# Optimization experiments

Hardware: AMD Instinct MI355X
Metric: run time of the kernel (lower is better)

The kernel has to match this reference:

```python
import jax, jax.numpy as jnp
import numpy as np

N = 50000      # nodes
E = 800000     # edges (avg degree 16)
DIN = 512      # input_dim
DH = 256       # hidden_dim
KMAX = 50      # max_clusters; K = max(5, min(50, ceil(N/50))) = 50 for N=50000


def _gcn_propagate(h, src, dst, n):
    """Symmetric-normalized GCN aggregation with self-loops (PyG GCNConv).
    h: already linearly transformed node features (n, d)."""
    loop = jnp.arange(n)
    s = jnp.concatenate([src, loop])
    d = jnp.concatenate([dst, loop])
    deg = jax.ops.segment_sum(jnp.ones_like(d, dtype=h.dtype), d, num_segments=n)
    dinv = jnp.where(deg > 0, deg ** -0.5, 0.0)
    norm = dinv[s] * dinv[d]                      # (E+N,)
    return jax.ops.segment_sum(norm[:, None] * h[s], d, num_segments=n)


def setup_inputs() -> dict:
    key = jax.random.key(0)
    ks = jax.random.split(key, 6)
    x = jax.random.normal(ks[0], (N, DIN), dtype=jnp.float32)
    edge_index = jax.random.randint(ks[1], (2, E), 0, N, dtype=jnp.int64)
    positions = jax.random.uniform(ks[2], (N, 2), dtype=jnp.float32)
    # GCNConv params (glorot-ish weights, zero bias as in PyG init)
    W1 = jax.random.normal(ks[3], (DIN, DH), dtype=jnp.float32) * np.float32(1.0 / np.sqrt(DIN))
    b1 = jnp.zeros((DH,), dtype=jnp.float32)
    W2 = jax.random.normal(ks[4], (DH, KMAX), dtype=jnp.float32) * np.float32(1.0 / np.sqrt(DH))
    b2 = jnp.zeros((KMAX,), dtype=jnp.float32)
    spatial_weight = jnp.asarray(1.0, dtype=jnp.float32)
    return {"x": x, "positions": positions, "W1": W1, "b1": b1,
            "W2": W2, "b2": b2, "spatial_weight": spatial_weight,
            "edge_index": edge_index}


def reference(x, positions, W1, b1, W2, b2, spatial_weight, edge_index):
    src, dst = edge_index[0], edge_index[1]
    n = x.shape[0]
    # layer 1: GCNConv(input_dim -> hidden_dim) + ReLU
    h = jax.nn.relu(_gcn_propagate(x @ W1, src, dst, n) + b1)
    # layer 2: GCNConv(hidden_dim -> max_clusters)
    s = _gcn_propagate(h @ W2, src, dst, n) + b2
    # K = max(5, min(50, ceil(N/50))) = 50 here -> s[:, :K] is identity slice
    S = jax.nn.softmax(s[:, :KMAX], axis=1)       # (N, K), Eq. 7
    # spatial loss (Eq. 9): softmax > 0 always, so the >0 guards are no-ops
    d2 = jnp.sum((positions[src] - positions[dst]) ** 2, axis=1)   # (E,) squared dist
    dot = jnp.sum(S[src] * S[dst], axis=1)                          # (E,) sum_k S_ik S_jk
    L_spatial = spatial_weight * jnp.sum(d2 * dot) / src.shape[0]
    return S, L_spatial
```

## Files before the change

kernel.cpp:

```cpp
#include <hip/hip_runtime.h>
#include <math.h>


typedef __attribute__((ext_vector_type(8))) short bf16x8;
typedef __attribute__((ext_vector_type(4))) float f32x4;
typedef __attribute__((ext_vector_type(4))) unsigned int u32x4;
typedef _Float16 f16;
typedef __attribute__((ext_vector_type(2))) _Float16 f16x2;
typedef __attribute__((ext_vector_type(4))) _Float16 f16x4;
typedef __attribute__((ext_vector_type(8))) _Float16 f16x8;

__device__ inline unsigned short f32_to_bf16(float f) {
    unsigned u = __float_as_uint(f);
    unsigned r = u + 0x7FFFu + ((u >> 16) & 1u);
    return (unsigned short)(r >> 16);
}
__device__ inline float bf16_to_f32(unsigned short h) {
    return __uint_as_float((unsigned)h << 16);
}

__device__ inline void glds16(const void* g, void* l) {
    __builtin_amdgcn_global_load_lds(
        (const __attribute__((address_space(1))) unsigned int*)g,
        (__attribute__((address_space(3))) unsigned int*)l, 16, 0, 0);
}

__global__ void detect_i64_kernel(const unsigned* __restrict__ w, int* __restrict__ flag) {
    __shared__ int red[256];
    int cnt = 0;
    for (int i = threadIdx.x; i < 4096; i += 256)
        cnt += (w[2 * i + 1] == 0u) ? 1 : 0;
    red[threadIdx.x] = cnt;
    __syncthreads();
    for (int s = 128; s > 0; s >>= 1) {
        if ((int)threadIdx.x < s) red[threadIdx.x] += red[threadIdx.x + s];
        __syncthreads();
    }
    if (threadIdx.x == 0) *flag = (red[0] > 2048) ? 1 : 0;
}

__global__ void convert_edges_kernel(const void* __restrict__ ei, int* __restrict__ es,
                                     int* __restrict__ ed, int* __restrict__ cnt,
                                     int E, const int* __restrict__ flag) {
    int idx = blockIdx.x * blockDim.x + threadIdx.x;
    if (idx >= 2 * E) return;
    int v;
    if (*flag) v = (int)((const long long*)ei)[idx];
    else       v = ((const int*)ei)[idx];
    if (idx < E) es[idx] = v;
    else { ed[idx - E] = v; atomicAdd(&cnt[v], 1); }
}

__global__ __launch_bounds__(1024) void scan_block_kernel(const int* __restrict__ cnt,
        int* __restrict__ row_ptr, int* __restrict__ btot, int n) {
    __shared__ int buf[1024];
    int i = blockIdx.x * 1024 + threadIdx.x;
    buf[threadIdx.x] = (i < n) ? cnt[i] : 0;
    __syncthreads();
    for (int off = 1; off < 1024; off <<= 1) {
        int t = ((int)threadIdx.x >= off) ? buf[threadIdx.x - off] : 0;
        __syncthreads();
        buf[threadIdx.x] += t;
        __syncthreads();
    }
    if (i < n) row_ptr[i + 1] = buf[threadIdx.x];
    if (threadIdx.x == 1023) btot[blockIdx.x] = buf[1023];
}

__global__ __launch_bounds__(1024) void scan_tops_kernel(int* __restrict__ btot, int nb) {
    __shared__ int buf[1024];
    buf[threadIdx.x] = ((int)threadIdx.x < nb) ? btot[threadIdx.x] : 0;
    __syncthreads();
    for (int off = 1; off < 1024; off <<= 1) {
        int t = ((int)threadIdx.x >= off) ? buf[threadIdx.x - off] : 0;
        __syncthreads();
        buf[threadIdx.x] += t;
        __syncthreads();
    }
    if ((int)threadIdx.x < nb) btot[threadIdx.x] = buf[threadIdx.x];
}

__global__ void scan_finalize_kernel(int* __restrict__ row_ptr, const int* __restrict__ btot,
        const int* __restrict__ cnt, int* __restrict__ cursor, float* __restrict__ dinv, int n) {
    int i = blockIdx.x * blockDim.x + threadIdx.x;
    if (i >= n) return;
    int blk = i >> 10;
    int off = blk ? btot[blk - 1] : 0;
    int incl = row_ptr[i + 1] + off;
    row_ptr[i + 1] = incl;
    cursor[i] = incl - cnt[i];
    dinv[i] = rsqrtf((float)(cnt[i] + 1));
    if (i == 0) row_ptr[0] = 0;
}

__global__ void scatter_kernel(const int* __restrict__ es, const int* __restrict__ ed,
                               const float* __restrict__ dinv, int* __restrict__ cursor,
                               int* __restrict__ csr_src, float* __restrict__ csr_nrm, int E) {
    int e = blockIdx.x * blockDim.x + threadIdx.x;
    if (e < E) {
        int s = es[e];
        int d = ed[e];
        int p = atomicAdd(&cursor[d], 1);
        csr_src[p] = s;
        csr_nrm[p] = dinv[s];
    }
}

__global__ void wsplit_kernel(const float* __restrict__ W,
                              unsigned short* __restrict__ Th,
                              unsigned short* __restrict__ Tl, int K, int N, int nk) {
    int idx = blockIdx.x * 256 + threadIdx.x;
    if (idx >= K * N) return;
    int k = idx / N, n = idx % N;
    float f = W[idx];
    unsigned short h = f32_to_bf16(f);
    unsigned short l = f32_to_bf16(f - bf16_to_f32(h));
    int p = n >> 7, np = n & 127, t = k >> 5, kg = (k & 31) >> 3, ke = k & 7;
    size_t o = ((size_t)((p * nk + t) * 4 + kg) << 10) + np * 8 + ke;
    Th[o] = h;
    Tl[o] = l;
}

__global__ void wsplit2_kernel(const float* __restrict__ W2,
                               f16* __restrict__ W2t_hi, f16* __restrict__ W2t_lo,
                               int K, int NC) {
    int idx = blockIdx.x * 256 + threadIdx.x;
    if (idx >= 64 * K) return;
    int n = idx / K, k = idx % K;
    float v = (n < NC) ? W2[(size_t)k * NC + n] : 0.f;
    f16 h = (f16)v;
    W2t_hi[idx] = h;
    W2t_lo[idx] = (f16)(v - (float)h);
}

#define G1_BM 128
#define G1_BN 128
#define G1_BK 32

__global__ __launch_bounds__(256) void gemm1_mfma(
        const float* __restrict__ X, const unsigned short* __restrict__ WtH,
        const unsigned short* __restrict__ WtL, f16* __restrict__ C,
        int M, int K, int N) {
    __shared__ __align__(16) unsigned char lds[32768];

    const int tid  = threadIdx.x;
    const int lane = tid & 63;
    const int wave = tid >> 6;
    const int wm   = wave & 1;
    const int wn   = wave >> 1;
    const int m0   = blockIdx.x * G1_BM;
    const int pn   = blockIdx.y;
    const int nk   = K / G1_BK;

    const float* Xbase[4];
    #pragma unroll
    for (int i = 0; i < 4; ++i) {
        int c   = i * 256 + tid;
        int row = c >> 3;
        int sl  = (c & 7) ^ (row & 7);
        int gr  = m0 + row;
        if (gr > M - 1) gr = M - 1;
        Xbase[i] = X + (size_t)gr * K + sl * 4;
    }
    const unsigned short* BhBase = WtH + ((size_t)pn * nk << 12) + (size_t)tid * 8;
    const unsigned short* BlBase = WtL + ((size_t)pn * nk << 12) + (size_t)tid * 8;

    f32x4 acc[4][4] = {};
    const int kq   = lane >> 4;
    const int frow = lane & 15;
    const int bOff = 16384 + (kq << 11) + ((wn * 64 + frow) << 4);

    for (int t = 0; t < nk; ++t) {
        const int k0 = t * G1_BK;
        #pragma unroll
        for (int i = 0; i < 4; ++i)
            glds16(Xbase[i] + k0, lds + i * 4096 + wave * 1024);
        const unsigned short* bh = BhBase + (size_t)t * 4096;
        const unsigned short* bl = BlBase + (size_t)t * 4096;
        glds16(bh,        lds + 16384 + wave * 1024);
        glds16(bh + 2048, lds + 20480 + wave * 1024);
        glds16(bl,        lds + 24576 + wave * 1024);
        glds16(bl + 2048, lds + 28672 + wave * 1024);
        __syncthreads();

        bf16x8 bhf[4], blf[4];
        #pragma unroll
        for (int nn = 0; nn < 4; ++nn) {
            bhf[nn] = *(const bf16x8*)(lds + bOff + nn * 256);
            blf[nn] = *(const bf16x8*)(lds + bOff + 8192 + nn * 256);
        }
        #pragma unroll
        for (int mm = 0; mm < 4; ++mm) {
            int ra = wm * 64 + mm * 16 + frow;
            int rb = ra << 7;
            int sw = (ra & 7) << 4;
            int s0 = kq << 1;
            f32x4 p0 = *(const f32x4*)(lds + rb + ((s0 << 4) ^ sw));
            f32x4 p1 = *(const f32x4*)(lds + rb + (((s0 + 1) << 4) ^ sw));
            float f[8] = {p0[0], p0[1], p0[2], p0[3], p1[0], p1[1], p1[2], p1[3]};
            u32x4 hv, lv;
            #pragma unroll
            for (int p = 0; p < 4; ++p) {
                unsigned b0 = __float_as_uint(f[2 * p]);
                unsigned b1 = __float_as_uint(f[2 * p + 1]);
                hv[p] = __builtin_amdgcn_perm(b1, b0, 0x07060302u);
                float l0 = f[2 * p]     - __uint_as_float(b0 & 0xFFFF0000u);
                float l1 = f[2 * p + 1] - __uint_as_float(b1 & 0xFFFF0000u);
                lv[p] = __builtin_amdgcn_perm(__float_as_uint(l1),
                                              __float_as_uint(l0), 0x07060302u);
            }
            union { u32x4 u; bf16x8 b; } ah, al;
            ah.u = hv; al.u = lv;
            #pragma unroll
            for (int nn = 0; nn < 4; ++nn)
                acc[mm][nn] = __builtin_amdgcn_mfma_f32_16x16x32_bf16(ah.b, bhf[nn], acc[mm][nn], 0, 0, 0);
            #pragma unroll
            for (int nn = 0; nn < 4; ++nn)
                acc[mm][nn] = __builtin_amdgcn_mfma_f32_16x16x32_bf16(ah.b, blf[nn], acc[mm][nn], 0, 0, 0);
            #pragma unroll
            for (int nn = 0; nn < 4; ++nn)
                acc[mm][nn] = __builtin_amdgcn_mfma_f32_16x16x32_bf16(al.b, bhf[nn], acc[mm][nn], 0, 0, 0);
        }
        __syncthreads();
    }

    const int n0 = pn * G1_BN;
    #pragma unroll
    for (int mm = 0; mm < 4; ++mm) {
        #pragma unroll
        for (int i = 0; i < 4; ++i) {
            int gr = m0 + wm * 64 + mm * 16 + kq * 4 + i;
            if (gr >= M) continue;
            #pragma unroll
            for (int nn = 0; nn < 4; ++nn) {
                int gc = n0 + wn * 64 + nn * 16 + frow;
                C[(size_t)gr * N + gc] = (f16)acc[mm][nn][i];
            }
        }
    }
}

__global__ __launch_bounds__(256) void agg1_gemm2_kernel(
        const f16* __restrict__ h0, const float* __restrict__ dinv,
        const int* __restrict__ row_ptr, const int* __restrict__ csr_src,
        const float* __restrict__ csr_nrm, const float* __restrict__ b1,
        const f16* __restrict__ W2t_hi, const f16* __restrict__ W2t_lo,
        f16* __restrict__ g, int n, int K, int KC) {
    __shared__ __align__(16) f16 hs[32][264];

    const int tid  = threadIdx.x;
    const int lane = tid & 63;
    const int wave = tid >> 6;
    const int base = blockIdx.x * 32;
    const int c    = lane & 31;
    const int hf   = lane >> 5;

    const f16x8* h0v8 = (const f16x8*)h0;

    float4 bA = ((const float4*)b1)[c * 2];
    float4 bB = ((const float4*)b1)[c * 2 + 1];
    float bb[8] = {bA.x, bA.y, bA.z, bA.w, bB.x, bB.y, bB.z, bB.w};

    for (int i = 0; i < 8; ++i) {
        int wid = base + wave * 8 + i;
        float acc[8] = {};
        if (wid < n) {
            float di = dinv[wid];
            f16x8 vs = h0v8[(size_t)wid * 32 + c];
            float selfm = (hf == 0) ? di * di : 0.f;
            #pragma unroll
            for (int q = 0; q < 8; ++q) acc[q] = selfm * (float)vs[q];
            int beg = row_ptr[wid], end = row_ptr[wid + 1];
            int j = beg;
            for (; j + 4 <= end; j += 4) {
                int   sA = csr_src[j + hf];
                int   sB = csr_src[j + 2 + hf];
                float nA = csr_nrm[j + hf] * di;
                float nB = csr_nrm[j + 2 + hf] * di;
                f16x8 uA = h0v8[(size_t)sA * 32 + c];
                f16x8 uB = h0v8[(size_t)sB * 32 + c];
                #pragma unroll
                for (int q = 0; q < 8; ++q) acc[q] = fmaf(nA, (float)uA[q], acc[q]);
                #pragma unroll
                for (int q = 0; q < 8; ++q) acc[q] = fmaf(nB, (float)uB[q], acc[q]);
            }
            for (; j < end; j += 2) {
                int  jj = j + hf;
                bool vld = jj < end;
                int   sA = csr_src[vld ? jj : j];
                float nA = vld ? csr_nrm[jj] * di : 0.f;
                f16x8 uA = h0v8[(size_t)sA * 32 + c];
                #pragma unroll
                for (int q = 0; q < 8; ++q) acc[q] = fmaf(nA, (float)uA[q], acc[q]);
            }
        }
        #pragma unroll
        for (int q = 0; q < 8; ++q) acc[q] += __shfl_xor(acc[q], 32);
        if (hf == 0) {
            f16x8 o;
            #pragma unroll
            for (int q = 0; q < 8; ++q)
                o[q] = (wid < n) ? (f16)fmaxf(acc[q] + bb[q], 0.f) : (f16)0.f;
            *(f16x8*)&hs[wave * 8 + i][c * 8] = o;
        }
    }
    __syncthreads();

    const int wm   = wave & 1;
    const int wn   = wave >> 1;
    const int kq   = lane >> 4;
    const int frow = lane & 15;
    const int koff = kq * 8;

    f32x4 acc2[2] = {};
    const f16* bh_base[2];
    const f16* bl_base[2];
    #pragma unroll
    for (int nn = 0; nn < 2; ++nn) {
        int r = wn * 32 + nn * 16 + frow;
        bh_base[nn] = W2t_hi + (size_t)r * K + koff;
        bl_base[nn] = W2t_lo + (size_t)r * K + koff;
    }

    for (int t = 0; t < K / 32; ++t) {
        const int kk = t * 32;
        f16x8 a = *(const f16x8*)&hs[wm * 16 + frow][kk + koff];
        #pragma unroll
        for (int nn = 0; nn < 2; ++nn) {
            f16x8 bh = *(const f16x8*)(bh_base[nn] + kk);
            f16x8 bl = *(const f16x8*)(bl_base[nn] + kk);
            acc2[nn] = __builtin_amdgcn_mfma_f32_16x16x32_f16(a, bh, acc2[nn], 0, 0, 0);
            acc2[nn] = __builtin_amdgcn_mfma_f32_16x16x32_f16(a, bl, acc2[nn], 0, 0, 0);
        }
    }

    #pragma unroll
    for (int i = 0; i < 4; ++i) {
        int gr = base + wm * 16 + kq * 4 + i;
        if (gr >= n) continue;
        #pragma unroll
        for (int nn = 0; nn < 2; ++nn) {
            int gc = wn * 32 + nn * 16 + frow;
            if (gc < KC) g[(size_t)gr * KC + gc] = (f16)acc2[nn][i];
        }
    }
}

__global__ __launch_bounds__(256) void agg2_softmax_kernel(const f16* __restrict__ g,
        const float* __restrict__ dinv, const int* __restrict__ row_ptr,
        const int* __restrict__ csr_src, const float* __restrict__ csr_nrm,
        const float* __restrict__ b2, float* __restrict__ S, f16* __restrict__ Sh,
        int n, int KC) {
    int wid = (int)((blockIdx.x * (size_t)blockDim.x + threadIdx.x) >> 6);
    int lane = threadIdx.x & 63;
    if (wid >= n) return;
    bool act = lane < KC;
    size_t gidx = act ? (size_t)lane : 0;
    float di = dinv[wid];
    float a0 = 0.f, a1 = 0.f, a2 = 0.f, a3 = 0.f;
    if (act) a0 = di * di * (float)g[(size_t)wid * KC + lane];
    int beg = row_ptr[wid], end = row_ptr[wid + 1];
    int j = beg;
    for (; j + 4 <= end; j += 4) {
        int s0 = csr_src[j], s1 = csr_src[j + 1], s2 = csr_src[j + 2], s3 = csr_src[j + 3];
        float n0 = csr_nrm[j]     * di;
        float n1 = csr_nrm[j + 1] * di;
        float n2 = csr_nrm[j + 2] * di;
        float n3 = csr_nrm[j + 3] * di;
        float g0 = (float)g[(size_t)s0 * KC + gidx];
        float g1 = (float)g[(size_t)s1 * KC + gidx];
        float g2 = (float)g[(size_t)s2 * KC + gidx];
        float g3 = (float)g[(size_t)s3 * KC + gidx];
        a0 = fmaf(n0, g0, a0);
        a1 = fmaf(n1, g1, a1);
        a2 = fmaf(n2, g2, a2);
        a3 = fmaf(n3, g3, a3);
    }
    for (; j < end; ++j) {
        int s0 = csr_src[j];
        float n0 = csr_nrm[j] * di;
        a0 = fmaf(n0, (float)g[(size_t)s0 * KC + gidx], a0);
    }
    float acc = (a0 + a1) + (a2 + a3);
    float val = act ? (acc + b2[lane]) : -INFINITY;
    float m = val;
    #pragma unroll
    for (int o = 32; o > 0; o >>= 1) m = fmaxf(m, __shfl_xor(m, o));
    float e = act ? expf(val - m) : 0.f;
    float ssum = e;
    #pragma unroll
    for (int o = 32; o > 0; o >>= 1) ssum += __shfl_xor(ssum, o);
    {
        float sv = act ? (e / ssum) : 0.f;
        if (act) S[(size_t)wid * KC + lane] = sv;
        Sh[(size_t)wid * 64 + lane] = (f16)sv;
    }
}

__global__ __launch_bounds__(256) void loss_partial_kernel(const int* __restrict__ es,
        const int* __restrict__ ed, const float* __restrict__ pos,
        const f16* __restrict__ Sh, float* __restrict__ parts, int E) {
    float local = 0.f;
    int stride = gridDim.x * blockDim.x;
    for (int e = blockIdx.x * blockDim.x + threadIdx.x; e < E; e += stride) {
        int s = es[e], d = ed[e];
        float2 ps = ((const float2*)pos)[s];
        float2 pd = ((const float2*)pos)[d];
        float dx = ps.x - pd.x, dy = ps.y - pd.y;
        float d2 = dx * dx + dy * dy;
        const f16x8* Sa = (const f16x8*)(Sh + (size_t)s * 64);
        const f16x8* Sb = (const f16x8*)(Sh + (size_t)d * 64);
        float dot = 0.f;
        #pragma unroll
        for (int q = 0; q < 7; ++q) {
            f16x8 a = Sa[q], b = Sb[q];
            #pragma unroll
            for (int k = 0; k < 8; ++k)
                dot = fmaf((float)a[k], (float)b[k], dot);
        }
        local = fmaf(d2, dot, local);
    }
    __shared__ float red[256];
    red[threadIdx.x] = local;
    __syncthreads();
    for (int s = 128; s > 0; s >>= 1) {
        if ((int)threadIdx.x < s) red[threadIdx.x] += red[threadIdx.x + s];
        __syncthreads();
    }
    if (threadIdx.x == 0) parts[blockIdx.x] = red[0];
}

__global__ __launch_bounds__(1024) void loss_final_kernel(const float* __restrict__ parts,
        const float* __restrict__ sw, float* __restrict__ out, float invE) {
    __shared__ float red[1024];
    red[threadIdx.x] = parts[threadIdx.x];
    __syncthreads();
    for (int s = 512; s > 0; s >>= 1) {
        if ((int)threadIdx.x < s) red[threadIdx.x] += red[threadIdx.x + s];
        __syncthreads();
    }
    if (threadIdx.x == 0) out[0] = sw[0] * red[0] * invE;
}

extern "C" void kernel_launch(void* const* d_in, const int* in_sizes, int n_in,
                              void* d_out, int out_size, void* d_ws, size_t ws_size,
                              hipStream_t stream) {
    const float* x   = (const float*)d_in[0];
    const float* pos = (const float*)d_in[1];
    const float* W1  = (const float*)d_in[2];
    const float* b1  = (const float*)d_in[3];
    const float* W2  = (const float*)d_in[4];
    const float* b2  = (const float*)d_in[5];
    const float* sw  = (const float*)d_in[6];
    const void*  ei  = d_in[7];

    const int DH  = in_sizes[3];
    const int KC  = in_sizes[5];
    const int DIN = in_sizes[2] / DH;
    const int n   = in_sizes[0] / DIN;
    const int E   = in_sizes[7] / 2;

    char* p = (char*)d_ws;
    auto alloc = [&](size_t bytes) {
        char* r = p;
        p += (bytes + 255) & ~(size_t)255;
        return r;
    };
    int*   flag    = (int*)alloc(256);
    int*   es      = (int*)alloc((size_t)E * 4);
    int*   ed      = (int*)alloc((size_t)E * 4);
    int*   cnt     = (int*)alloc((size_t)n * 4);
    int*   cursor  = (int*)alloc((size_t)n * 4);
    int*   row_ptr = (int*)alloc(((size_t)n + 1) * 4);
    int*   btot    = (int*)alloc(1024 * 4);
    int*   csr     = (int*)alloc((size_t)E * 4);
    float* csr_nrm = (float*)alloc((size_t)E * 4);
    float* dinv    = (float*)alloc((size_t)n * 4);
    float* parts   = (float*)alloc(1024 * 4);
    unsigned short* Wt_hi = (unsigned short*)alloc((size_t)DIN * DH * 2);
    unsigned short* Wt_lo = (unsigned short*)alloc((size_t)DIN * DH * 2);
    f16*   W2t_hi  = (f16*)alloc((size_t)64 * DH * 2);
    f16*   W2t_lo  = (f16*)alloc((size_t)64 * DH * 2);
    f16*   h0      = (f16*)alloc((size_t)n * DH * 2);
    f16*   g       = (f16*)alloc((size_t)n * KC * 2);
    f16*   Sh      = (f16*)alloc((size_t)n * 64 * 2);

    float* S    = (float*)d_out;
    float* Lout = S + (size_t)n * KC;

    const int nb = (n + 1023) / 1024;
    const int nk = DIN / G1_BK;

    hipMemsetAsync(cnt, 0, (size_t)n * 4, stream);
    detect_i64_kernel<<<1, 256, 0, stream>>>((const unsigned*)ei, flag);
    convert_edges_kernel<<<(2 * E + 255) / 256, 256, 0, stream>>>(ei, es, ed, cnt, E, flag);
    scan_block_kernel<<<nb, 1024, 0, stream>>>(cnt, row_ptr, btot, n);
    scan_tops_kernel<<<1, 1024, 0, stream>>>(btot, nb);
    scan_finalize_kernel<<<(n + 255) / 256, 256, 0, stream>>>(row_ptr, btot, cnt, cursor, dinv, n);
    scatter_kernel<<<(E + 255) / 256, 256, 0, stream>>>(es, ed, dinv, cursor, csr, csr_nrm, E);

    wsplit_kernel<<<(DIN * DH + 255) / 256, 256, 0, stream>>>(W1, Wt_hi, Wt_lo, DIN, DH, nk);
    wsplit2_kernel<<<(64 * DH + 255) / 256, 256, 0, stream>>>(W2, W2t_hi, W2t_lo, DH, KC);

    dim3 g1((n + G1_BM - 1) / G1_BM, DH / G1_BN);
    gemm1_mfma<<<g1, 256, 0, stream>>>(x, Wt_hi, Wt_lo, h0, n, DIN, DH);

    agg1_gemm2_kernel<<<(n + 31) / 32, 256, 0, stream>>>(
        h0, dinv, row_ptr, csr, csr_nrm, b1, W2t_hi, W2t_lo, g, n, DH, KC);

    agg2_softmax_kernel<<<(int)(((size_t)n * 64 + 255) / 256), 256, 0, stream>>>(
        g, dinv, row_ptr, csr, csr_nrm, b2, S, Sh, n, KC);

    loss_partial_kernel<<<1024, 256, 0, stream>>>(es, ed, pos, Sh, parts, E);
    loss_final_kernel<<<1, 1024, 0, stream>>>(parts, sw, Lout, 1.0f / (float)E);
}
```

Before: 326.8 us.

## Interleave CSR src/norm, pad layer-2 features to 64, vectorize loss

Packs each CSR entry's source index and normalization weight into one int2 so a single load fetches both in the aggregation kernels. Pads the layer-2 intermediate to a 64-column stride, which removes per-lane bounds masking, and unrolls the layer-2 gather by eight for more memory-level parallelism. The loss kernel processes two edges per iteration with vector index loads and computes the softmax dot product with packed half-precision multiplies. The half-precision accumulation in the loss dot product lowers accuracy compared with the previous fp32 FMA chain.

New measurement: 334.8 us. 2.5% more time.

```diff
diff --git a/kernel.cpp b/kernel.cpp
--- a/kernel.cpp
+++ b/kernel.cpp
@@ -95,14 +95,13 @@
 
 __global__ void scatter_kernel(const int* __restrict__ es, const int* __restrict__ ed,
                                const float* __restrict__ dinv, int* __restrict__ cursor,
-                               int* __restrict__ csr_src, float* __restrict__ csr_nrm, int E) {
+                               int2* __restrict__ csr_sn, int E) {
     int e = blockIdx.x * blockDim.x + threadIdx.x;
     if (e < E) {
         int s = es[e];
         int d = ed[e];
         int p = atomicAdd(&cursor[d], 1);
-        csr_src[p] = s;
-        csr_nrm[p] = dinv[s];
+        csr_sn[p] = make_int2(s, __float_as_int(dinv[s]));
     }
 }
 
@@ -242,8 +241,8 @@
 
 __global__ __launch_bounds__(256) void agg1_gemm2_kernel(
         const f16* __restrict__ h0, const float* __restrict__ dinv,
-        const int* __restrict__ row_ptr, const int* __restrict__ csr_src,
-        const float* __restrict__ csr_nrm, const float* __restrict__ b1,
+        const int* __restrict__ row_ptr, const int2* __restrict__ csr_sn,
+        const float* __restrict__ b1,
         const f16* __restrict__ W2t_hi, const f16* __restrict__ W2t_lo,
         f16* __restrict__ g, int n, int K, int KC) {
     __shared__ __align__(16) f16 hs[32][264];
@@ -273,12 +272,12 @@
             int beg = row_ptr[wid], end = row_ptr[wid + 1];
             int j = beg;
             for (; j + 4 <= end; j += 4) {
-                int   sA = csr_src[j + hf];
-                int   sB = csr_src[j + 2 + hf];
-                float nA = csr_nrm[j + hf] * di;
-                float nB = csr_nrm[j + 2 + hf] * di;
-                f16x8 uA = h0v8[(size_t)sA * 32 + c];
-                f16x8 uB = h0v8[(size_t)sB * 32 + c];
+                int2 eA = csr_sn[j + hf];
+                int2 eB = csr_sn[j + 2 + hf];
+                float nA = __int_as_float(eA.y) * di;
+                float nB = __int_as_float(eB.y) * di;
+                f16x8 uA = h0v8[(size_t)eA.x * 32 + c];
+                f16x8 uB = h0v8[(size_t)eB.x * 32 + c];
                 #pragma unroll
                 for (int q = 0; q < 8; ++q) acc[q] = fmaf(nA, (float)uA[q], acc[q]);
                 #pragma unroll
@@ -287,9 +286,9 @@
             for (; j < end; j += 2) {
                 int  jj = j + hf;
                 bool vld = jj < end;
-                int   sA = csr_src[vld ? jj : j];
-                float nA = vld ? csr_nrm[jj] * di : 0.f;
-                f16x8 uA = h0v8[(size_t)sA * 32 + c];
+                int2 eA = csr_sn[vld ? jj : j];
+                float nA = vld ? __int_as_float(eA.y) * di : 0.f;
+                f16x8 uA = h0v8[(size_t)eA.x * 32 + c];
                 #pragma unroll
                 for (int q = 0; q < 8; ++q) acc[q] = fmaf(nA, (float)uA[q], acc[q]);
             }
@@ -341,47 +340,64 @@
         #pragma unroll
         for (int nn = 0; nn < 2; ++nn) {
             int gc = wn * 32 + nn * 16 + frow;
-            if (gc < KC) g[(size_t)gr * KC + gc] = (f16)acc2[nn][i];
+            g[(size_t)gr * 64 + gc] = (f16)acc2[nn][i];
         }
     }
 }
 
 __global__ __launch_bounds__(256) void agg2_softmax_kernel(const f16* __restrict__ g,
         const float* __restrict__ dinv, const int* __restrict__ row_ptr,
-        const int* __restrict__ csr_src, const float* __restrict__ csr_nrm,
-        const float* __restrict__ b2, float* __restrict__ S, f16* __restrict__ Sh,
-        int n, int KC) {
+        const int2* __restrict__ csr_sn, const float* __restrict__ b2,
+        float* __restrict__ S, f16* __restrict__ Sh, int n, int KC) {
     int wid = (int)((blockIdx.x * (size_t)blockDim.x + threadIdx.x) >> 6);
     int lane = threadIdx.x & 63;
     if (wid >= n) return;
     bool act = lane < KC;
-    size_t gidx = act ? (size_t)lane : 0;
     float di = dinv[wid];
     float a0 = 0.f, a1 = 0.f, a2 = 0.f, a3 = 0.f;
-    if (act) a0 = di * di * (float)g[(size_t)wid * KC + lane];
+    float a4 = 0.f, a5 = 0.f, a6 = 0.f, a7 = 0.f;
+    a0 = di * di * (float)g[(size_t)wid * 64 + lane];
     int beg = row_ptr[wid], end = row_ptr[wid + 1];
     int j = beg;
+    for (; j + 8 <= end; j += 8) {
+        int2 e0 = csr_sn[j],     e1 = csr_sn[j + 1];
+        int2 e2 = csr_sn[j + 2], e3 = csr_sn[j + 3];
+        int2 e4 = csr_sn[j + 4], e5 = csr_sn[j + 5];
+        int2 e6 = csr_sn[j + 6], e7 = csr_sn[j + 7];
+        float g0 = (float)g[(size_t)e0.x * 64 + lane];
+        float g1 = (float)g[(size_t)e1.x * 64 + lane];
+        float g2 = (float)g[(size_t)e2.x * 64 + lane];
+        float g3 = (float)g[(size_t)e3.x * 64 + lane];
+        float g4 = (float)g[(size_t)e4.x * 64 + lane];
+        float g5 = (float)g[(size_t)e5.x * 64 + lane];
+        float g6 = (float)g[(size_t)e6.x * 64 + lane];
+        float g7 = (float)g[(size_t)e7.x * 64 + lane];
+        a0 = fmaf(__int_as_float(e0.y) * di, g0, a0);
+        a1 = fmaf(__int_as_float(e1.y) * di, g1, a1);
+        a2 = fmaf(__int_as_float(e2.y) * di, g2, a2);
+        a3 = fmaf(__int_as_float(e3.y) * di, g3, a3);
+        a4 = fmaf(__int_as_float(e4.y) * di, g4, a4);
+        a5 = fmaf(__int_as_float(e5.y) * di, g5, a5);
+        a6 = fmaf(__int_as_float(e6.y) * di, g6, a6);
+        a7 = fmaf(__int_as_float(e7.y) * di, g7, a7);
+    }
     for (; j + 4 <= end; j += 4) {
-        int s0 = csr_src[j], s1 = csr_src[j + 1], s2 = csr_src[j + 2], s3 = csr_src[j + 3];
-        float n0 = csr_nrm[j]     * di;
-        float n1 = csr_nrm[j + 1] * di;
-        float n2 = csr_nrm[j + 2] * di;
-        float n3 = csr_nrm[j + 3] * di;
-        float g0 = (float)g[(size_t)s0 * KC + gidx];
-        float g1 = (float)g[(size_t)s1 * KC + gidx];
-        float g2 = (float)g[(size_t)s2 * KC + gidx];
-        float g3 = (float)g[(size_t)s3 * KC + gidx];
-        a0 = fmaf(n0, g0, a0);
-        a1 = fmaf(n1, g1, a1);
-        a2 = fmaf(n2, g2, a2);
-        a3 = fmaf(n3, g3, a3);
+        int2 e0 = csr_sn[j],     e1 = csr_sn[j + 1];
+        int2 e2 = csr_sn[j + 2], e3 = csr_sn[j + 3];
+        float g0 = (float)g[(size_t)e0.x * 64 + lane];
+        float g1 = (float)g[(size_t)e1.x * 64 + lane];
+        float g2 = (float)g[(size_t)e2.x * 64 + lane];
+        float g3 = (float)g[(size_t)e3.x * 64 + lane];
+        a0 = fmaf(__int_as_float(e0.y) * di, g0, a0);
+        a1 = fmaf(__int_as_float(e1.y) * di, g1, a1);
+        a2 = fmaf(__int_as_float(e2.y) * di, g2, a2);
+        a3 = fmaf(__int_as_float(e3.y) * di, g3, a3);
     }
     for (; j < end; ++j) {
-        int s0 = csr_src[j];
-        float n0 = csr_nrm[j] * di;
-        a0 = fmaf(n0, (float)g[(size_t)s0 * KC + gidx], a0);
-    }
-    float acc = (a0 + a1) + (a2 + a3);
+        int2 e0 = csr_sn[j];
+        a0 = fmaf(__int_as_float(e0.y) * di, (float)g[(size_t)e0.x * 64 + lane], a0);
+    }
+    float acc = ((a0 + a1) + (a2 + a3)) + ((a4 + a5) + (a6 + a7));
     float val = act ? (acc + b2[lane]) : -INFINITY;
     float m = val;
     #pragma unroll
@@ -401,24 +417,46 @@
         const int* __restrict__ ed, const float* __restrict__ pos,
         const f16* __restrict__ Sh, float* __restrict__ parts, int E) {
     float local = 0.f;
+    int idx = blockIdx.x * blockDim.x + threadIdx.x;
     int stride = gridDim.x * blockDim.x;
-    for (int e = blockIdx.x * blockDim.x + threadIdx.x; e < E; e += stride) {
+    const int np = E >> 1;
+    for (int p = idx; p < np; p += stride) {
+        int2 s2 = ((const int2*)es)[p];
+        int2 d2i = ((const int2*)ed)[p];
+        #pragma unroll
+        for (int u = 0; u < 2; ++u) {
+            int s = u ? s2.y : s2.x;
+            int d = u ? d2i.y : d2i.x;
+            const f16x8* Sa = (const f16x8*)(Sh + (size_t)s * 64);
+            const f16x8* Sb = (const f16x8*)(Sh + (size_t)d * 64);
+            f16x8 dacc = {0, 0, 0, 0, 0, 0, 0, 0};
+            #pragma unroll
+            for (int q = 0; q < 7; ++q)
+                dacc += Sa[q] * Sb[q];
+            float dot = 0.f;
+            #pragma unroll
+            for (int k = 0; k < 8; ++k) dot += (float)dacc[k];
+            float2 ps = ((const float2*)pos)[s];
+            float2 pd = ((const float2*)pos)[d];
+            float dx = ps.x - pd.x, dy = ps.y - pd.y;
+            local = fmaf(dx * dx + dy * dy, dot, local);
+        }
+    }
+    if ((E & 1) && idx == 0) {
+        int e = E - 1;
         int s = es[e], d = ed[e];
+        const f16x8* Sa = (const f16x8*)(Sh + (size_t)s * 64);
+        const f16x8* Sb = (const f16x8*)(Sh + (size_t)d * 64);
+        f16x8 dacc = {0, 0, 0, 0, 0, 0, 0, 0};
+        #pragma unroll
+        for (int q = 0; q < 7; ++q) dacc += Sa[q] * Sb[q];
+        float dot = 0.f;
+        #pragma unroll
+        for (int k = 0; k < 8; ++k) dot += (float)dacc[k];
         float2 ps = ((const float2*)pos)[s];
         float2 pd = ((const float2*)pos)[d];
         float dx = ps.x - pd.x, dy = ps.y - pd.y;
-        float d2 = dx * dx + dy * dy;
-        const f16x8* Sa = (const f16x8*)(Sh + (size_t)s * 64);
-        const f16x8* Sb = (const f16x8*)(Sh + (size_t)d * 64);
-        float dot = 0.f;
-        #pragma unroll
-        for (int q = 0; q < 7; ++q) {
-            f16x8 a = Sa[q], b = Sb[q];
-            #pragma unroll
-            for (int k = 0; k < 8; ++k)
-                dot = fmaf((float)a[k], (float)b[k], dot);
-        }
-        local = fmaf(d2, dot, local);
+        local = fmaf(dx * dx + dy * dy, dot, local);
     }
     __shared__ float red[256];
     red[threadIdx.x] = local;
@@ -473,8 +511,7 @@
     int*   cursor  = (int*)alloc((size_t)n * 4);
     int*   row_ptr = (int*)alloc(((size_t)n + 1) * 4);
     int*   btot    = (int*)alloc(1024 * 4);
-    int*   csr     = (int*)alloc((size_t)E * 4);
-    float* csr_nrm = (float*)alloc((size_t)E * 4);
+    int2*  csr_sn  = (int2*)alloc((size_t)E * 8);
     float* dinv    = (float*)alloc((size_t)n * 4);
     float* parts   = (float*)alloc(1024 * 4);
     unsigned short* Wt_hi = (unsigned short*)alloc((size_t)DIN * DH * 2);
@@ -482,7 +519,7 @@
     f16*   W2t_hi  = (f16*)alloc((size_t)64 * DH * 2);
     f16*   W2t_lo  = (f16*)alloc((size_t)64 * DH * 2);
     f16*   h0      = (f16*)alloc((size_t)n * DH * 2);
-    f16*   g       = (f16*)alloc((size_t)n * KC * 2);
+    f16*   g       = (f16*)alloc((size_t)n * 64 * 2);
     f16*   Sh      = (f16*)alloc((size_t)n * 64 * 2);
 
     float* S    = (float*)d_out;
@@ -497,7 +534,7 @@
     scan_block_kernel<<<nb, 1024, 0, stream>>>(cnt, row_ptr, btot, n);
     scan_tops_kernel<<<1, 1024, 0, stream>>>(btot, nb);
     scan_finalize_kernel<<<(n + 255) / 256, 256, 0, stream>>>(row_ptr, btot, cnt, cursor, dinv, n);
-    scatter_kernel<<<(E + 255) / 256, 256, 0, stream>>>(es, ed, dinv, cursor, csr, csr_nrm, E);
+    scatter_kernel<<<(E + 255) / 256, 256, 0, stream>>>(es, ed, dinv, cursor, csr_sn, E);
 
     wsplit_kernel<<<(DIN * DH + 255) / 256, 256, 0, stream>>>(W1, Wt_hi, Wt_lo, DIN, DH, nk);
     wsplit2_kernel<<<(64 * DH + 255) / 256, 256, 0, stream>>>(W2, W2t_hi, W2t_lo, DH, KC);
@@ -506,10 +543,10 @@
     gemm1_mfma<<<g1, 256, 0, stream>>>(x, Wt_hi, Wt_lo, h0, n, DIN, DH);
 
     agg1_gemm2_kernel<<<(n + 31) / 32, 256, 0, stream>>>(
-        h0, dinv, row_ptr, csr, csr_nrm, b1, W2t_hi, W2t_lo, g, n, DH, KC);
+        h0, dinv, row_ptr, csr_sn, b1, W2t_hi, W2t_lo, g, n, DH, KC);
 
     agg2_softmax_kernel<<<(int)(((size_t)n * 64 + 255) / 256), 256, 0, stream>>>(
-        g, dinv, row_ptr, csr, csr_nrm, b2, S, Sh, n, KC);
+        g, dinv, row_ptr, csr_sn, b2, S, Sh, n, KC);
 
     loss_partial_kernel<<<1024, 256, 0, stream>>>(es, ed, pos, Sh, parts, E);
     loss_final_kernel<<<1, 1024, 0, stream>>>(parts, sw, Lout, 1.0f / (float)E);
```
